# Kernel tuning notes

Hardware: AMD Instinct MI355X
Metric: run time of the kernel (lower is better)

## Reference

```python
import jax, jax.numpy as jnp
import numpy as np

B, WIN, NIN, H, NOUT = 256, 100, 700, 512, 20
MAXD, STRIDE = 40, 4
ND = MAXD // STRIDE          # len(delays) = 10
THRESH = 0.3                 # thresh == output_thresh in this config


def _spike(x):
    # forward of surrogate-gradient ActFun: Heaviside(x)
    return (x > 0).astype(x.dtype)


def setup_inputs() -> dict:
    key = jax.random.key(0)
    ks = jax.random.split(key, 7)
    def lin(k, out_f, in_f):  # torch nn.Linear default init U(-1/sqrt(in), 1/sqrt(in))
        lim = 1.0 / np.sqrt(in_f)
        return jax.random.uniform(k, (out_f, in_f), minval=-lim, maxval=lim, dtype=jnp.float32)
    return {
        "input": jax.random.uniform(ks[0], (B, WIN, NIN), dtype=jnp.float32),
        "W0": lin(ks[1], H, NIN),            # f0_i: input -> layer1 current (no delays)
        "W1": lin(ks[2], H, H * ND),         # f1_f2: delayed spikes -> layer2
        "Wo": lin(ks[3], NOUT, H * ND),      # f2_o: delayed spikes -> output
        "tau1": jax.random.normal(ks[4], (H,), dtype=jnp.float32),
        "tau2": jax.random.normal(ks[5], (H,), dtype=jnp.float32),
        "tau_o": jax.random.normal(ks[6], (NOUT,), dtype=jnp.float32),
    }


def _delayed(buf):
    # buf: (MAXD, B, H) holds spikes of steps t-MAXD .. t-1.
    # torch reads extended[:, t+d, :] for d in range(0, MAXD, STRIDE) = steps t-MAXD+d,
    # then .transpose(1,2).reshape(B, -1) -> (B, H*ND) with delay fastest axis.
    sel = buf[::STRIDE]                        # (ND, B, H)
    return jnp.transpose(sel, (1, 2, 0)).reshape(B, H * ND)


def _forward(input, W0, W1, Wo, tau1, tau2, tau_o):
    a1, a2, ao = jax.nn.sigmoid(tau1), jax.nn.sigmoid(tau2), jax.nn.sigmoid(tau_o)

    def step(carry, x_t):
        mem1, s1, mem2, s2, o_mem, o_spk, buf1, buf2, o_sum, out_mot = carry
        # layer 1: current is f0_i(x) directly (h_layers[0] == Identity)
        mem1 = mem1 * a1 * (1.0 - s1) + x_t @ W0.T
        s1 = _spike(mem1 - THRESH)
        mem1 = jnp.where(mem1 < THRESH, mem1, 0.0)
        prev1 = _delayed(buf1)                              # read before appending step-t spike
        buf1 = jnp.concatenate([buf1[1:], s1[None]], axis=0)
        # layer 2
        mem2 = mem2 * a2 * (1.0 - s2) + prev1 @ W1.T
        s2 = _spike(mem2 - THRESH)
        mem2 = jnp.where(mem2 < THRESH, mem2, 0.0)
        prev2 = _delayed(buf2)
        buf2 = jnp.concatenate([buf2[1:], s2[None]], axis=0)
        # output layer
        o_mem = o_mem * ao * (1.0 - o_spk) + prev2 @ Wo.T
        o_spk = _spike(o_mem - THRESH)
        o_mem = jnp.where(o_mem < THRESH, o_mem, 0.0)
        o_sum = o_sum + o_spk
        out_mot = out_mot + jax.nn.softmax(o_mem, axis=1)
        return (mem1, s1, mem2, s2, o_mem, o_spk, buf1, buf2, o_sum, out_mot), None

    z_h = jnp.zeros((B, H), jnp.float32)
    z_o = jnp.zeros((B, NOUT), jnp.float32)
    z_buf = jnp.zeros((MAXD, B, H), jnp.float32)
    carry0 = (z_h, z_h, z_h, z_h, z_o, z_o, z_buf, z_buf, z_o, z_o)
    carry, _ = jax.lax.scan(step, carry0, jnp.transpose(input, (1, 0, 2)))
    o_sum, out_mot = carry[8], carry[9]
    return o_sum / WIN, out_mot


def reference(input, W0, W1, Wo, tau1, tau2, tau_o):
    return _forward(input, W0, W1, Wo, tau1, tau2, tau_o)
```

## Files before the change

kernel.cpp:

```cpp
#include <hip/hip_runtime.h>
#include <stdint.h>

#define THRESH_ 0.3f
constexpr int B_ = 256, WIN_ = 100, NIN_ = 700, NINP_ = 704, H_ = 512;
constexpr int NOUT_ = 20, NOUTP_ = 32, ND_ = 10, KBIG_ = 5120, M_ = 25600;
constexpr int PLANES_ = 140;

typedef unsigned short u16;
typedef unsigned int u32;
typedef unsigned short u16x4 __attribute__((ext_vector_type(4)));
typedef unsigned short u16x8 __attribute__((ext_vector_type(8)));
typedef float f32x4 __attribute__((ext_vector_type(4)));

__device__ __forceinline__ u16 f2h(float f) {
  _Float16 h = (_Float16)f;
  union { _Float16 h; u16 u; } v; v.h = h;
  return v.u;
}
__device__ __forceinline__ float h2f(u16 u) {
  union { u16 u; _Float16 h; } v; v.u = u;
  return (float)v.h;
}

__device__ __forceinline__ void mfma_h(f32x4& acc, u16x8 a, u16x8 b) {
  asm volatile("v_mfma_f32_16x16x32_f16 %0, %1, %2, %0" : "+v"(acc) : "v"(a), "v"(b));
}
__device__ __forceinline__ void gload16(const void* g, void* l) {
  __builtin_amdgcn_global_load_lds(
      (const __attribute__((address_space(1))) unsigned int*)g,
      (__attribute__((address_space(3))) unsigned int*)l, 16, 0, 0);
}


__global__ __launch_bounds__(256) void k_split_x(const float* __restrict__ in,
                                                 u16* __restrict__ xh, u16* __restrict__ xl) {
  int r = blockIdx.x * 4 + (threadIdx.x >> 6);
  int l = threadIdx.x & 63;
  int t = r >> 8, b = r & 255;
  const f32x4* src = (const f32x4*)(in + (size_t)(b * WIN_ + t) * NIN_);
  u16x4* dh = (u16x4*)(xh + (size_t)r * NINP_);
  u16x4* dl = (u16x4*)(xl + (size_t)r * NINP_);
#pragma unroll
  for (int i = 0; i < 3; i++) {
    int k4 = l + 64 * i;
    if (k4 < 176) {
      f32x4 v = (k4 < 175) ? src[k4] : (f32x4){0.f, 0.f, 0.f, 0.f};
      u16x4 hh, ll;
#pragma unroll
      for (int e = 0; e < 4; e++) {
        u16 h = f2h(v[e]);
        hh[e] = h;
        ll[e] = f2h(v[e] - h2f(h));
      }
      dh[k4] = hh;
      dl[k4] = ll;
    }
  }
}


__global__ __launch_bounds__(256) void k_prep_w(const float* __restrict__ W0,
                                                const float* __restrict__ W1,
                                                const float* __restrict__ Wo,
                                                u16* __restrict__ w0h, u16* __restrict__ w0l,
                                                u16* __restrict__ w1h, u16* __restrict__ w1l,
                                                u16* __restrict__ woh, u16* __restrict__ wol) {
  int bid = blockIdx.x;
  if (bid < 512) {
    int j = bid;
#pragma unroll
    for (int i = 0; i < 3; i++) {
      int k = threadIdx.x + 256 * i;
      if (k < NINP_) {
        float v = (k < NIN_) ? W0[j * NIN_ + k] * 256.0f : 0.f;
        u16 h = f2h(v);
        u16 lo = f2h(v - h2f(h));
        w0h[j * NINP_ + k] = h;
        w0l[j * NINP_ + k] = lo;
      }
    }
  } else if (bid < 1024) {
    int j = bid - 512;
#pragma unroll 1
    for (int i = 0; i < 20; i++) {
      int k = threadIdx.x + 256 * i;
      int d = k >> 9, h = k & 511;
      float v = W1[(size_t)j * KBIG_ + h * ND_ + d] * 256.0f;
      u16 a = f2h(v);
      u16 b = f2h(v - h2f(a));
      w1h[(size_t)j * KBIG_ + k] = a;
      w1l[(size_t)j * KBIG_ + k] = b;
    }
  } else {
    int j = bid - 1024;
#pragma unroll 1
    for (int i = 0; i < 20; i++) {
      int k = threadIdx.x + 256 * i;
      int d = k >> 9, h = k & 511;
      float v = (j < NOUT_) ? Wo[(size_t)j * KBIG_ + h * ND_ + d] * 256.0f : 0.f;
      u16 a = f2h(v);
      u16 b = f2h(v - h2f(a));
      woh[(size_t)j * KBIG_ + k] = a;
      wol[(size_t)j * KBIG_ + k] = b;
    }
  }
}


__global__ __launch_bounds__(256) void k_gemm0(const u16* __restrict__ Xh, const u16* __restrict__ Xl,
                                               const u16* __restrict__ Wh, const u16* __restrict__ Wl,
                                               float* __restrict__ out) {
  __shared__ alignas(16) u16 lAh[128 * 32], lAl[128 * 32], lBh[128 * 32], lBl[128 * 32];
  const int tid = threadIdx.x, lane = tid & 63, wid = tid >> 6;
  const int m0 = blockIdx.x * 128, n0 = blockIdx.y * 128;
  const int wr = wid >> 1, wc = wid & 1;
  const int srow = lane >> 2;
  const int sk = 8 * ((lane & 3) ^ ((lane >> 3) & 3));
  const int fr = lane & 15, kb = lane >> 4;
  int aoff[4], boff[4];
#pragma unroll
  for (int f = 0; f < 4; f++) {
    int row = wr * 64 + f * 16 + fr;
    aoff[f] = row * 32 + (kb ^ ((row >> 1) & 3)) * 8;
    int col = wc * 64 + f * 16 + fr;
    boff[f] = col * 32 + (kb ^ ((col >> 1) & 3)) * 8;
  }
  f32x4 acc[4][4] = {};
#pragma unroll 1
  for (int kk = 0; kk < NINP_ / 32; kk++) {
    const int k0 = kk * 32;
#pragma unroll
    for (int i = 0; i < 2; i++) {
      int c = wid + 4 * i;
      int ga = (m0 + c * 16 + srow) * NINP_ + k0 + sk;
      gload16(Xh + ga, &lAh[c * 512]);
      gload16(Xl + ga, &lAl[c * 512]);
      int gb = (n0 + c * 16 + srow) * NINP_ + k0 + sk;
      gload16(Wh + gb, &lBh[c * 512]);
      gload16(Wl + gb, &lBl[c * 512]);
    }
    asm volatile("s_waitcnt vmcnt(0)" ::: "memory");
    __syncthreads();
    u16x8 bh[4], bl[4];
#pragma unroll
    for (int j = 0; j < 4; j++) {
      bh[j] = *(const u16x8*)&lBh[boff[j]];
      bl[j] = *(const u16x8*)&lBl[boff[j]];
    }
#pragma unroll
    for (int i = 0; i < 4; i++) {
      u16x8 ah = *(const u16x8*)&lAh[aoff[i]];
      u16x8 al = *(const u16x8*)&lAl[aoff[i]];
#pragma unroll
      for (int j = 0; j < 4; j++) {
        mfma_h(acc[i][j], ah, bh[j]);
        mfma_h(acc[i][j], ah, bl[j]);
        mfma_h(acc[i][j], al, bh[j]);
      }
    }
    __syncthreads();
  }
  asm volatile("s_nop 7\n\ts_nop 7" ::: "memory");
#pragma unroll
  for (int i = 0; i < 4; i++) {
    int row = m0 + wr * 64 + i * 16 + (lane >> 4) * 4;
#pragma unroll
    for (int j = 0; j < 4; j++) {
      int col = n0 + wc * 64 + j * 16 + fr;
#pragma unroll
      for (int r = 0; r < 4; r++)
        out[(row + r) * H_ + col] = acc[i][j][r] * (1.0f / 256.0f);
    }
  }
}


__global__ __launch_bounds__(256) void k_gemm_spk(const u16* __restrict__ S, const u16* __restrict__ Wh,
                                                  const u16* __restrict__ Wl, float* __restrict__ out) {
  __shared__ alignas(16) u16 lA[128 * 64], lBh[128 * 64], lBl[128 * 64];
  const int tid = threadIdx.x, lane = tid & 63, wid = tid >> 6;
  const int mt = blockIdx.x;
  const int m0 = mt * 128, n0 = blockIdx.y * 128;
  const int t = mt >> 1, brow0 = (mt & 1) * 128;
  const int wr = wid >> 1, wc = wid & 1;
  const int srow8 = lane >> 3;
  const int ksrc = ((lane >> 2) & 1) * 32 + 8 * ((lane & 3) ^ ((lane >> 4) & 3));
  const int fr = lane & 15, kb = lane >> 4;
  const int kx = (kb ^ ((fr >> 1) & 3)) * 8;
  int aoff[4], boff[4];
#pragma unroll
  for (int f = 0; f < 4; f++) {
    aoff[f] = (wr * 64 + f * 16 + fr) * 64 + kx;
    boff[f] = (wc * 64 + f * 16 + fr) * 64 + kx;
  }
  f32x4 acc[4][4] = {};
#pragma unroll 1
  for (int kk = 0; kk < KBIG_ / 64; kk++) {
    const int k0 = kk * 64;
    const int d = k0 >> 9, h0 = k0 & 511;
    const int p = t + 4 * d;
    const u16* Sb = S + (size_t)(p * 256 + brow0) * 512 + h0 + ksrc;
#pragma unroll
    for (int c = 0; c < 4; c++) {
      int rb = c * 32 + wid * 8;
      gload16(Sb + (rb + srow8) * 512, &lA[rb * 64]);
      size_t gb = (size_t)(n0 + rb + srow8) * KBIG_ + k0 + ksrc;
      gload16(Wh + gb, &lBh[rb * 64]);
      gload16(Wl + gb, &lBl[rb * 64]);
    }
    asm volatile("s_waitcnt vmcnt(0)" ::: "memory");
    __syncthreads();
#pragma unroll
    for (int s = 0; s < 2; s++) {
      const int so = s * 32;
      u16x8 bh[4], bl[4];
#pragma unroll
      for (int j = 0; j < 4; j++) {
        bh[j] = *(const u16x8*)&lBh[boff[j] + so];
        bl[j] = *(const u16x8*)&lBl[boff[j] + so];
      }
#pragma unroll
      for (int i = 0; i < 4; i++) {
        u16x8 a = *(const u16x8*)&lA[aoff[i] + so];
#pragma unroll
        for (int j = 0; j < 4; j++) {
          mfma_h(acc[i][j], a, bh[j]);
          mfma_h(acc[i][j], a, bl[j]);
        }
      }
    }
    __syncthreads();
  }
  asm volatile("s_nop 7\n\ts_nop 7" ::: "memory");
#pragma unroll
  for (int i = 0; i < 4; i++) {
    int row = m0 + wr * 64 + i * 16 + (lane >> 4) * 4;
#pragma unroll
    for (int j = 0; j < 4; j++) {
      int col = n0 + wc * 64 + j * 16 + fr;
#pragma unroll
      for (int r = 0; r < 4; r++)
        out[(row + r) * H_ + col] = acc[i][j][r] * (1.0f / 256.0f);
    }
  }
}


__global__ __launch_bounds__(256) void k_gemm_out(const u16* __restrict__ S, const u16* __restrict__ Wh,
                                                  const u16* __restrict__ Wl, float* __restrict__ out) {
  __shared__ alignas(16) u16 lA[128 * 64], lBh[32 * 64], lBl[32 * 64];
  const int tid = threadIdx.x, lane = tid & 63, wid = tid >> 6;
  const int mt = blockIdx.x;
  const int m0 = mt * 128;
  const int t = mt >> 1, brow0 = (mt & 1) * 128;
  const int srow8 = lane >> 3;
  const int ksrc = ((lane >> 2) & 1) * 32 + 8 * ((lane & 3) ^ ((lane >> 4) & 3));
  const int fr = lane & 15, kb = lane >> 4;
  const int kx = (kb ^ ((fr >> 1) & 3)) * 8;
  int aoff[2], boff[2];
#pragma unroll
  for (int f = 0; f < 2; f++) {
    aoff[f] = (wid * 32 + f * 16 + fr) * 64 + kx;
    boff[f] = (f * 16 + fr) * 64 + kx;
  }
  f32x4 acc[2][2] = {};
#pragma unroll 1
  for (int kk = 0; kk < KBIG_ / 64; kk++) {
    const int k0 = kk * 64;
    const int d = k0 >> 9, h0 = k0 & 511;
    const int p = t + 4 * d;
    const u16* Sb = S + (size_t)(p * 256 + brow0) * 512 + h0 + ksrc;
#pragma unroll
    for (int c = 0; c < 4; c++) {
      int rb = c * 32 + wid * 8;
      gload16(Sb + (rb + srow8) * 512, &lA[rb * 64]);
    }
    gload16(Wh + (size_t)(wid * 8 + srow8) * KBIG_ + k0 + ksrc, &lBh[(wid * 8) * 64]);
    gload16(Wl + (size_t)(wid * 8 + srow8) * KBIG_ + k0 + ksrc, &lBl[(wid * 8) * 64]);
    asm volatile("s_waitcnt vmcnt(0)" ::: "memory");
    __syncthreads();
#pragma unroll
    for (int s = 0; s < 2; s++) {
      const int so = s * 32;
      u16x8 bh[2], bl[2];
#pragma unroll
      for (int j = 0; j < 2; j++) {
        bh[j] = *(const u16x8*)&lBh[boff[j] + so];
        bl[j] = *(const u16x8*)&lBl[boff[j] + so];
      }
#pragma unroll
      for (int i = 0; i < 2; i++) {
        u16x8 a = *(const u16x8*)&lA[aoff[i] + so];
#pragma unroll
        for (int j = 0; j < 2; j++) {
          mfma_h(acc[i][j], a, bh[j]);
          mfma_h(acc[i][j], a, bl[j]);
        }
      }
    }
    __syncthreads();
  }
  asm volatile("s_nop 7\n\ts_nop 7" ::: "memory");
#pragma unroll
  for (int i = 0; i < 2; i++) {
    int row = m0 + wid * 32 + i * 16 + (lane >> 4) * 4;
#pragma unroll
    for (int j = 0; j < 2; j++) {
      int col = j * 16 + fr;
#pragma unroll
      for (int r = 0; r < 4; r++)
        out[(row + r) * NOUTP_ + col] = acc[i][j][r] * (1.0f / 256.0f);
    }
  }
}


__global__ void k_scan(const float* __restrict__ cur, const float* __restrict__ tau, u16* __restrict__ S) {
  int g = blockIdx.x * 256 + threadIdx.x;
  int b = g >> 9, h = g & 511;
  float a = (float)(1.0 / (1.0 + exp(-(double)tau[h])));
  float mem = 0.f, s = 0.f;
#pragma unroll 1
  for (int tt = 0; tt < 20; tt++) {
    float c[5];
#pragma unroll
    for (int q = 0; q < 5; q++)
      c[q] = cur[((tt * 5 + q) * 256 + b) * 512 + h];
    u16 sv[5];
#pragma unroll
    for (int q = 0; q < 5; q++) {
      mem = __fadd_rn(__fmul_rn(__fmul_rn(mem, a), __fsub_rn(1.f, s)), c[q]);
      float x = __fsub_rn(mem, THRESH_);
      s = (x > 0.f) ? 1.f : 0.f;
      mem = (mem < THRESH_) ? mem : 0.f;
      sv[q] = (x > 0.f) ? (u16)0x3C00 : (u16)0;
    }
#pragma unroll
    for (int q = 0; q < 5; q++)
      S[((tt * 5 + q + 40) * 256 + b) * 512 + h] = sv[q];
  }
}

__global__ void k_scan_o(const float* __restrict__ curo, const float* __restrict__ tau, float* __restrict__ outp) {
  int b = blockIdx.x * 64 + threadIdx.x;
  if (b >= B_) return;
  float ao[NOUT_], mem[NOUT_], spk[NOUT_], osum[NOUT_], mot[NOUT_];
#pragma unroll
  for (int j = 0; j < NOUT_; j++) {
    ao[j] = (float)(1.0 / (1.0 + exp(-(double)tau[j])));
    mem[j] = 0.f; spk[j] = 0.f; osum[j] = 0.f; mot[j] = 0.f;
  }
#pragma unroll 1
  for (int t = 0; t < WIN_; t++) {
    const float4* rowp = (const float4*)&curo[(t * 256 + b) * NOUTP_];
    float4 v[5];
#pragma unroll
    for (int q = 0; q < 5; q++) v[q] = rowp[q];
    float cv[NOUT_];
#pragma unroll
    for (int q = 0; q < 5; q++) {
      cv[4 * q + 0] = v[q].x; cv[4 * q + 1] = v[q].y;
      cv[4 * q + 2] = v[q].z; cv[4 * q + 3] = v[q].w;
    }
#pragma unroll
    for (int j = 0; j < NOUT_; j++) {
      mem[j] = __fadd_rn(__fmul_rn(__fmul_rn(mem[j], ao[j]), __fsub_rn(1.f, spk[j])), cv[j]);
      float x = __fsub_rn(mem[j], THRESH_);
      spk[j] = (x > 0.f) ? 1.f : 0.f;
      mem[j] = (mem[j] < THRESH_) ? mem[j] : 0.f;
      osum[j] = __fadd_rn(osum[j], spk[j]);
    }
    float mx = -1e30f;
#pragma unroll
    for (int j = 0; j < NOUT_; j++) mx = fmaxf(mx, mem[j]);
    float se = 0.f, e[NOUT_];
#pragma unroll
    for (int j = 0; j < NOUT_; j++) { e[j] = expf(__fsub_rn(mem[j], mx)); se = __fadd_rn(se, e[j]); }
#pragma unroll
    for (int j = 0; j < NOUT_; j++) mot[j] = __fadd_rn(mot[j], __fdiv_rn(e[j], se));
  }
#pragma unroll
  for (int j = 0; j < NOUT_; j++) {
    outp[b * NOUT_ + j] = __fdiv_rn(osum[j], 100.0f);
    outp[B_ * NOUT_ + b * NOUT_ + j] = mot[j];
  }
}


extern "C" void kernel_launch(void* const* d_in, const int* in_sizes, int n_in,
                              void* d_out, int out_size, void* d_ws, size_t ws_size,
                              hipStream_t stream) {
  const float* in   = (const float*)d_in[0];
  const float* W0   = (const float*)d_in[1];
  const float* W1   = (const float*)d_in[2];
  const float* Wo   = (const float*)d_in[3];
  const float* tau1 = (const float*)d_in[4];
  const float* tau2 = (const float*)d_in[5];
  const float* tauo = (const float*)d_in[6];
  float* out = (float*)d_out;

  char* ws = (char*)d_ws;
  size_t off = 0;
  auto take = [&](size_t bytes) -> char* {
    char* p = ws + off;
    off += (bytes + 255) & ~(size_t)255;
    return p;
  };
  char* region0 = take((size_t)2 * M_ * NINP_ * 2);
  u16* Xh  = (u16*)region0;
  u16* Xl  = (u16*)(region0 + (size_t)M_ * NINP_ * 2);
  float* cur2 = (float*)region0;
  char* region1 = take((size_t)M_ * H_ * 4);
  float* cur1 = (float*)region1;
  u16* S2 = (u16*)region1;
  u16* W0h = (u16*)take((size_t)H_ * NINP_ * 2);
  u16* W0l = (u16*)take((size_t)H_ * NINP_ * 2);
  u16* W1h = (u16*)take((size_t)H_ * KBIG_ * 2);
  u16* W1l = (u16*)take((size_t)H_ * KBIG_ * 2);
  u16* Woh = (u16*)take((size_t)NOUTP_ * KBIG_ * 2);
  u16* Wol = (u16*)take((size_t)NOUTP_ * KBIG_ * 2);
  float* curo = (float*)take((size_t)M_ * NOUTP_ * 4);
  u16* S1 = (u16*)take((size_t)PLANES_ * B_ * H_ * 2);

  hipMemsetAsync(S1, 0, (size_t)40 * B_ * H_ * 2, stream);

  k_prep_w<<<dim3(1056), 256, 0, stream>>>(W0, W1, Wo, W0h, W0l, W1h, W1l, Woh, Wol);
  k_split_x<<<dim3(M_ / 4), 256, 0, stream>>>(in, Xh, Xl);

  k_gemm0<<<dim3(200, 4), 256, 0, stream>>>(Xh, Xl, W0h, W0l, cur1);
  k_scan<<<dim3(512), 256, 0, stream>>>(cur1, tau1, S1);
  hipMemsetAsync(S2, 0, (size_t)40 * B_ * H_ * 2, stream);
  k_gemm_spk<<<dim3(200, 4), 256, 0, stream>>>(S1, W1h, W1l, cur2);
  k_scan<<<dim3(512), 256, 0, stream>>>(cur2, tau2, S2);
  k_gemm_out<<<dim3(200), 256, 0, stream>>>(S2, Woh, Wol, curo);
  k_scan_o<<<dim3(4), 64, 0, stream>>>(curo, tauo, out);
}
```

Baseline: 638.2 us.

## Fuse prep kernels and memsets, parallelize output scan, shrink gemm_out tiles

```diff
diff --git a/kernel.cpp b/kernel.cpp
--- a/kernel.cpp
+++ b/kernel.cpp
@@ -32,42 +32,42 @@
 }
 
 
-__global__ __launch_bounds__(256) void k_split_x(const float* __restrict__ in,
-                                                 u16* __restrict__ xh, u16* __restrict__ xl) {
-  int r = blockIdx.x * 4 + (threadIdx.x >> 6);
-  int l = threadIdx.x & 63;
-  int t = r >> 8, b = r & 255;
-  const f32x4* src = (const f32x4*)(in + (size_t)(b * WIN_ + t) * NIN_);
-  u16x4* dh = (u16x4*)(xh + (size_t)r * NINP_);
-  u16x4* dl = (u16x4*)(xl + (size_t)r * NINP_);
-#pragma unroll
-  for (int i = 0; i < 3; i++) {
-    int k4 = l + 64 * i;
-    if (k4 < 176) {
-      f32x4 v = (k4 < 175) ? src[k4] : (f32x4){0.f, 0.f, 0.f, 0.f};
-      u16x4 hh, ll;
-#pragma unroll
-      for (int e = 0; e < 4; e++) {
-        u16 h = f2h(v[e]);
-        hh[e] = h;
-        ll[e] = f2h(v[e] - h2f(h));
-      }
-      dh[k4] = hh;
-      dl[k4] = ll;
-    }
-  }
-}
-
-
-__global__ __launch_bounds__(256) void k_prep_w(const float* __restrict__ W0,
-                                                const float* __restrict__ W1,
-                                                const float* __restrict__ Wo,
-                                                u16* __restrict__ w0h, u16* __restrict__ w0l,
-                                                u16* __restrict__ w1h, u16* __restrict__ w1l,
-                                                u16* __restrict__ woh, u16* __restrict__ wol) {
+__global__ __launch_bounds__(256) void k_prep(const float* __restrict__ in,
+                                              const float* __restrict__ W0,
+                                              const float* __restrict__ W1,
+                                              const float* __restrict__ Wo,
+                                              u16* __restrict__ xh, u16* __restrict__ xl,
+                                              u16* __restrict__ w0h, u16* __restrict__ w0l,
+                                              u16* __restrict__ w1h, u16* __restrict__ w1l,
+                                              u16* __restrict__ woh, u16* __restrict__ wol,
+                                              u16* __restrict__ S1, u16* __restrict__ S2) {
+  __shared__ u16 lh[5120], ll[5120];
   int bid = blockIdx.x;
-  if (bid < 512) {
-    int j = bid;
+  if (bid < 6400) {
+    int r = bid * 4 + (threadIdx.x >> 6);
+    int l = threadIdx.x & 63;
+    int t = r >> 8, b = r & 255;
+    const f32x4* src = (const f32x4*)(in + (size_t)(b * WIN_ + t) * NIN_);
+    u16x4* dh = (u16x4*)(xh + (size_t)r * NINP_);
+    u16x4* dl = (u16x4*)(xl + (size_t)r * NINP_);
+#pragma unroll
+    for (int i = 0; i < 3; i++) {
+      int k4 = l + 64 * i;
+      if (k4 < 176) {
+        f32x4 v = (k4 < 175) ? src[k4] : (f32x4){0.f, 0.f, 0.f, 0.f};
+        u16x4 hh, lo;
+#pragma unroll
+        for (int e = 0; e < 4; e++) {
+          u16 h = f2h(v[e]);
+          hh[e] = h;
+          lo[e] = f2h(v[e] - h2f(h));
+        }
+        dh[k4] = hh;
+        dl[k4] = lo;
+      }
+    }
+  } else if (bid < 6912) {
+    int j = bid - 6400;
 #pragma unroll
     for (int i = 0; i < 3; i++) {
       int k = threadIdx.x + 256 * i;
@@ -79,20 +79,36 @@
         w0l[j * NINP_ + k] = lo;
       }
     }
-  } else if (bid < 1024) {
-    int j = bid - 512;
-#pragma unroll 1
-    for (int i = 0; i < 20; i++) {
-      int k = threadIdx.x + 256 * i;
-      int d = k >> 9, h = k & 511;
-      float v = W1[(size_t)j * KBIG_ + h * ND_ + d] * 256.0f;
-      u16 a = f2h(v);
-      u16 b = f2h(v - h2f(a));
-      w1h[(size_t)j * KBIG_ + k] = a;
-      w1l[(size_t)j * KBIG_ + k] = b;
-    }
-  } else {
-    int j = bid - 1024;
+  } else if (bid < 7424) {
+    int j = bid - 6912;
+#pragma unroll
+    for (int i = 0; i < 2; i++) {
+      int h = threadIdx.x + 256 * i;
+      const float* src = W1 + (size_t)j * KBIG_ + h * ND_;
+      float v[10];
+#pragma unroll
+      for (int q = 0; q < 5; q++) {
+        float2 p = *(const float2*)(src + 2 * q);
+        v[2 * q] = p.x; v[2 * q + 1] = p.y;
+      }
+#pragma unroll
+      for (int d = 0; d < 10; d++) {
+        float w = v[d] * 256.0f;
+        u16 a = f2h(w);
+        u16 c = f2h(w - h2f(a));
+        lh[d * 512 + h] = a;
+        ll[d * 512 + h] = c;
+      }
+    }
+    __syncthreads();
+#pragma unroll
+    for (int i = 0; i < 5; i++) {
+      int k4 = threadIdx.x + 256 * i;
+      *(u16x4*)&w1h[(size_t)j * KBIG_ + k4 * 4] = *(const u16x4*)&lh[k4 * 4];
+      *(u16x4*)&w1l[(size_t)j * KBIG_ + k4 * 4] = *(const u16x4*)&ll[k4 * 4];
+    }
+  } else if (bid < 7456) {
+    int j = bid - 7424;
 #pragma unroll 1
     for (int i = 0; i < 20; i++) {
       int k = threadIdx.x + 256 * i;
@@ -103,6 +119,13 @@
       woh[(size_t)j * KBIG_ + k] = a;
       wol[(size_t)j * KBIG_ + k] = b;
     }
+  } else {
+    u16* dst = (bid < 7616) ? S1 : S2;
+    int b0 = (bid < 7616) ? bid - 7456 : bid - 7616;
+    f32x4* p = (f32x4*)dst;
+#pragma unroll
+    for (int it = 0; it < 16; it++)
+      p[(size_t)(b0 * 16 + it) * 256 + threadIdx.x] = (f32x4){0.f, 0.f, 0.f, 0.f};
   }
 }
 
@@ -248,22 +271,20 @@
 
 __global__ __launch_bounds__(256) void k_gemm_out(const u16* __restrict__ S, const u16* __restrict__ Wh,
                                                   const u16* __restrict__ Wl, float* __restrict__ out) {
-  __shared__ alignas(16) u16 lA[128 * 64], lBh[32 * 64], lBl[32 * 64];
+  __shared__ alignas(16) u16 lA[64 * 64], lBh[32 * 64], lBl[32 * 64];
   const int tid = threadIdx.x, lane = tid & 63, wid = tid >> 6;
   const int mt = blockIdx.x;
-  const int m0 = mt * 128;
-  const int t = mt >> 1, brow0 = (mt & 1) * 128;
+  const int m0 = mt * 64;
+  const int t = mt >> 2, brow0 = (mt & 3) * 64;
   const int srow8 = lane >> 3;
   const int ksrc = ((lane >> 2) & 1) * 32 + 8 * ((lane & 3) ^ ((lane >> 4) & 3));
   const int fr = lane & 15, kb = lane >> 4;
   const int kx = (kb ^ ((fr >> 1) & 3)) * 8;
-  int aoff[2], boff[2];
-#pragma unroll
-  for (int f = 0; f < 2; f++) {
-    aoff[f] = (wid * 32 + f * 16 + fr) * 64 + kx;
-    boff[f] = (f * 16 + fr) * 64 + kx;
-  }
-  f32x4 acc[2][2] = {};
+  const int aoff = (wid * 16 + fr) * 64 + kx;
+  int boff[2];
+#pragma unroll
+  for (int f = 0; f < 2; f++) boff[f] = (f * 16 + fr) * 64 + kx;
+  f32x4 acc[2] = {};
 #pragma unroll 1
   for (int kk = 0; kk < KBIG_ / 64; kk++) {
     const int k0 = kk * 64;
@@ -271,7 +292,7 @@
     const int p = t + 4 * d;
     const u16* Sb = S + (size_t)(p * 256 + brow0) * 512 + h0 + ksrc;
 #pragma unroll
-    for (int c = 0; c < 4; c++) {
+    for (int c = 0; c < 2; c++) {
       int rb = c * 32 + wid * 8;
       gload16(Sb + (rb + srow8) * 512, &lA[rb * 64]);
     }
@@ -282,34 +303,26 @@
 #pragma unroll
     for (int s = 0; s < 2; s++) {
       const int so = s * 32;
-      u16x8 bh[2], bl[2];
+      u16x8 a = *(const u16x8*)&lA[aoff + so];
 #pragma unroll
       for (int j = 0; j < 2; j++) {
-        bh[j] = *(const u16x8*)&lBh[boff[j] + so];
-        bl[j] = *(const u16x8*)&lBl[boff[j] + so];
-      }
-#pragma unroll
-      for (int i = 0; i < 2; i++) {
-        u16x8 a = *(const u16x8*)&lA[aoff[i] + so];
-#pragma unroll
-        for (int j = 0; j < 2; j++) {
-          mfma_h(acc[i][j], a, bh[j]);
-          mfma_h(acc[i][j], a, bl[j]);
-        }
+        u16x8 bh = *(const u16x8*)&lBh[boff[j] + so];
+        u16x8 bl = *(const u16x8*)&lBl[boff[j] + so];
+        mfma_h(acc[j], a, bh);
+        mfma_h(acc[j], a, bl);
       }
     }
     __syncthreads();
   }
   asm volatile("s_nop 7\n\ts_nop 7" ::: "memory");
-#pragma unroll
-  for (int i = 0; i < 2; i++) {
-    int row = m0 + wid * 32 + i * 16 + (lane >> 4) * 4;
+  {
+    int row = m0 + wid * 16 + (lane >> 4) * 4;
 #pragma unroll
     for (int j = 0; j < 2; j++) {
       int col = j * 16 + fr;
 #pragma unroll
       for (int r = 0; r < 4; r++)
-        out[(row + r) * NOUTP_ + col] = acc[i][j][r] * (1.0f / 256.0f);
+        out[(row + r) * NOUTP_ + col] = acc[j][r] * (1.0f / 256.0f);
     }
   }
 }
@@ -321,14 +334,14 @@
   float a = (float)(1.0 / (1.0 + exp(-(double)tau[h])));
   float mem = 0.f, s = 0.f;
 #pragma unroll 1
-  for (int tt = 0; tt < 20; tt++) {
-    float c[5];
-#pragma unroll
-    for (int q = 0; q < 5; q++)
-      c[q] = cur[((tt * 5 + q) * 256 + b) * 512 + h];
-    u16 sv[5];
-#pragma unroll
-    for (int q = 0; q < 5; q++) {
+  for (int tt = 0; tt < 10; tt++) {
+    float c[10];
+#pragma unroll
+    for (int q = 0; q < 10; q++)
+      c[q] = cur[((tt * 10 + q) * 256 + b) * 512 + h];
+    u16 sv[10];
+#pragma unroll
+    for (int q = 0; q < 10; q++) {
       mem = __fadd_rn(__fmul_rn(__fmul_rn(mem, a), __fsub_rn(1.f, s)), c[q]);
       float x = __fsub_rn(mem, THRESH_);
       s = (x > 0.f) ? 1.f : 0.f;
@@ -336,53 +349,38 @@
       sv[q] = (x > 0.f) ? (u16)0x3C00 : (u16)0;
     }
 #pragma unroll
-    for (int q = 0; q < 5; q++)
-      S[((tt * 5 + q + 40) * 256 + b) * 512 + h] = sv[q];
+    for (int q = 0; q < 10; q++)
+      S[((tt * 10 + q + 40) * 256 + b) * 512 + h] = sv[q];
   }
 }
 
 __global__ void k_scan_o(const float* __restrict__ curo, const float* __restrict__ tau, float* __restrict__ outp) {
-  int b = blockIdx.x * 64 + threadIdx.x;
-  if (b >= B_) return;
-  float ao[NOUT_], mem[NOUT_], spk[NOUT_], osum[NOUT_], mot[NOUT_];
-#pragma unroll
-  for (int j = 0; j < NOUT_; j++) {
-    ao[j] = (float)(1.0 / (1.0 + exp(-(double)tau[j])));
-    mem[j] = 0.f; spk[j] = 0.f; osum[j] = 0.f; mot[j] = 0.f;
-  }
+  int tid = threadIdx.x;
+  int b = blockIdx.x * 8 + (tid >> 5);
+  int lj = tid & 31;
+  bool act = lj < NOUT_;
+  float ao = 0.f, mem = 0.f, spk = 0.f, osum = 0.f, mot = 0.f;
+  if (act) ao = (float)(1.0 / (1.0 + exp(-(double)tau[lj])));
 #pragma unroll 1
   for (int t = 0; t < WIN_; t++) {
-    const float4* rowp = (const float4*)&curo[(t * 256 + b) * NOUTP_];
-    float4 v[5];
-#pragma unroll
-    for (int q = 0; q < 5; q++) v[q] = rowp[q];
-    float cv[NOUT_];
-#pragma unroll
-    for (int q = 0; q < 5; q++) {
-      cv[4 * q + 0] = v[q].x; cv[4 * q + 1] = v[q].y;
-      cv[4 * q + 2] = v[q].z; cv[4 * q + 3] = v[q].w;
-    }
-#pragma unroll
-    for (int j = 0; j < NOUT_; j++) {
-      mem[j] = __fadd_rn(__fmul_rn(__fmul_rn(mem[j], ao[j]), __fsub_rn(1.f, spk[j])), cv[j]);
-      float x = __fsub_rn(mem[j], THRESH_);
-      spk[j] = (x > 0.f) ? 1.f : 0.f;
-      mem[j] = (mem[j] < THRESH_) ? mem[j] : 0.f;
-      osum[j] = __fadd_rn(osum[j], spk[j]);
-    }
-    float mx = -1e30f;
-#pragma unroll
-    for (int j = 0; j < NOUT_; j++) mx = fmaxf(mx, mem[j]);
-    float se = 0.f, e[NOUT_];
-#pragma unroll
-    for (int j = 0; j < NOUT_; j++) { e[j] = expf(__fsub_rn(mem[j], mx)); se = __fadd_rn(se, e[j]); }
-#pragma unroll
-    for (int j = 0; j < NOUT_; j++) mot[j] = __fadd_rn(mot[j], __fdiv_rn(e[j], se));
-  }
-#pragma unroll
-  for (int j = 0; j < NOUT_; j++) {
-    outp[b * NOUT_ + j] = __fdiv_rn(osum[j], 100.0f);
-    outp[B_ * NOUT_ + b * NOUT_ + j] = mot[j];
+    float cv = act ? curo[(size_t)(t * 256 + b) * NOUTP_ + lj] : 0.f;
+    mem = __fadd_rn(__fmul_rn(__fmul_rn(mem, ao), __fsub_rn(1.f, spk)), cv);
+    float x = __fsub_rn(mem, THRESH_);
+    spk = (x > 0.f) ? 1.f : 0.f;
+    mem = (mem < THRESH_) ? mem : 0.f;
+    if (act) osum = __fadd_rn(osum, spk);
+    float mx = act ? mem : -1e30f;
+#pragma unroll
+    for (int m = 16; m >= 1; m >>= 1) mx = fmaxf(mx, __shfl_xor(mx, m, 32));
+    float e = act ? expf(__fsub_rn(mem, mx)) : 0.f;
+    float se = e;
+#pragma unroll
+    for (int m = 16; m >= 1; m >>= 1) se = __fadd_rn(se, __shfl_xor(se, m, 32));
+    if (act) mot = __fadd_rn(mot, __fdiv_rn(e, se));
+  }
+  if (act) {
+    outp[b * NOUT_ + lj] = __fdiv_rn(osum, 100.0f);
+    outp[B_ * NOUT_ + b * NOUT_ + lj] = mot;
   }
 }
 
@@ -410,9 +408,7 @@
   u16* Xh  = (u16*)region0;
   u16* Xl  = (u16*)(region0 + (size_t)M_ * NINP_ * 2);
   float* cur2 = (float*)region0;
-  char* region1 = take((size_t)M_ * H_ * 4);
-  float* cur1 = (float*)region1;
-  u16* S2 = (u16*)region1;
+  float* cur1 = (float*)take((size_t)M_ * H_ * 4);
   u16* W0h = (u16*)take((size_t)H_ * NINP_ * 2);
   u16* W0l = (u16*)take((size_t)H_ * NINP_ * 2);
   u16* W1h = (u16*)take((size_t)H_ * KBIG_ * 2);
@@ -421,17 +417,15 @@
   u16* Wol = (u16*)take((size_t)NOUTP_ * KBIG_ * 2);
   float* curo = (float*)take((size_t)M_ * NOUTP_ * 4);
   u16* S1 = (u16*)take((size_t)PLANES_ * B_ * H_ * 2);
-
-  hipMemsetAsync(S1, 0, (size_t)40 * B_ * H_ * 2, stream);
-
-  k_prep_w<<<dim3(1056), 256, 0, stream>>>(W0, W1, Wo, W0h, W0l, W1h, W1l, Woh, Wol);
-  k_split_x<<<dim3(M_ / 4), 256, 0, stream>>>(in, Xh, Xl);
+  u16* S2 = (u16*)take((size_t)PLANES_ * B_ * H_ * 2);
+
+  k_prep<<<dim3(7776), 256, 0, stream>>>(in, W0, W1, Wo, Xh, Xl, W0h, W0l,
+                                         W1h, W1l, Woh, Wol, S1, S2);
 
   k_gemm0<<<dim3(200, 4), 256, 0, stream>>>(Xh, Xl, W0h, W0l, cur1);
   k_scan<<<dim3(512), 256, 0, stream>>>(cur1, tau1, S1);
-  hipMemsetAsync(S2, 0, (size_t)40 * B_ * H_ * 2, stream);
   k_gemm_spk<<<dim3(200, 4), 256, 0, stream>>>(S1, W1h, W1l, cur2);
   k_scan<<<dim3(512), 256, 0, stream>>>(cur2, tau2, S2);
-  k_gemm_out<<<dim3(200), 256, 0, stream>>>(S2, Woh, Wol, curo);
-  k_scan_o<<<dim3(4), 64, 0, stream>>>(curo, tauo, out);
-}
+  k_gemm_out<<<dim3(400), 256, 0, stream>>>(S2, Woh, Wol, curo);
+  k_scan_o<<<dim3(32), 256, 0, stream>>>(curo, tauo, out);
+}
```

Measured after the change: 522.5 us. 18.1% less time.
